# Kernel tuning notes

Hardware: AMD Instinct MI355X
Metric: run time of the kernel (lower is better)

## Reference

```python
import jax, jax.numpy as jnp
import numpy as np

NU, NI, E = 20000, 8000, 64
DV, DT = 4096, 768
NE, B = 200000, 4096
L_HET, L_HOMO = 2, 1
K_ISG, K_UCG = 10, 20
MMW, WD = 0.1, 1e-4


def setup_inputs() -> dict:
    ks = jax.random.split(jax.random.key(0), 14)
    return {
        "feat_v": jax.random.normal(ks[0], (NI, DV), jnp.float32),
        "feat_t": jax.random.normal(ks[1], (NI, DT), jnp.float32),
        "pref_v": jax.random.normal(ks[2], (NU, E), jnp.float32) * 0.1,
        "pref_t": jax.random.normal(ks[3], (NU, E), jnp.float32) * 0.1,
        "W_v": jax.random.normal(ks[4], (DV, E), jnp.float32) * 0.02,
        "W_t": jax.random.normal(ks[5], (DT, E), jnp.float32) * 0.02,
        "user_v_alpha": jax.random.normal(ks[6], (1,), jnp.float32),
        "user_nb_weights": jax.random.normal(ks[7], (NU, K_UCG), jnp.float32),
        "edge_users": jax.random.randint(ks[8], (NE,), 0, NU, jnp.int32),
        "edge_items": jax.random.randint(ks[9], (NE,), 0, NI, jnp.int32),
        "u_ids": jax.random.randint(ks[10], (B,), 0, NU, jnp.int32),
        "pos_ids": jax.random.randint(ks[11], (B,), 0, NI, jnp.int32),
        "neg_ids": jax.random.randint(ks[12], (B,), 0, NI, jnp.int32),
        "user_nb": jax.random.randint(ks[13], (NU, K_UCG), 0, NU, jnp.int32),
    }


def reference(feat_v, feat_t, pref_v, pref_t, W_v, W_t, user_v_alpha,
              user_nb_weights, edge_users, edge_items, u_ids, pos_ids,
              neg_ids, user_nb):
    N = NU + NI
    # bidirectional bipartite edges (items offset by NU)
    src = jnp.concatenate([edge_users, edge_items + NU])
    dst = jnp.concatenate([edge_items + NU, edge_users])
    deg = jax.ops.segment_sum(jnp.ones_like(src, jnp.float32), dst, num_segments=N)
    deg = jnp.maximum(deg, 1.0)
    norm = (1.0 / jnp.sqrt(deg[src] * deg[dst]))[:, None]

    def hetero_gcn(feat, pref, W):
        x = jnp.concatenate([pref, feat @ W], axis=0)  # [N, E]
        h, out = x, x
        for _ in range(L_HET):
            h = jax.ops.segment_sum(h[src] * norm, dst, num_segments=N)
            out = out + h
        return out[:NU], out[NU:]

    u_v, i_v = hetero_gcn(feat_v, pref_v, W_v)
    u_t, i_t = hetero_gcn(feat_t, pref_t, W_t)
    a_v = jax.nn.sigmoid(user_v_alpha[0])
    u_f = jnp.concatenate([a_v * u_v, (1.0 - a_v) * u_t], axis=1)  # [NU, 2E]
    i_f = jnp.concatenate([i_v, i_t], axis=1)                      # [NI, 2E]

    # Item Semantic Graph: KNN over cosine sim, no grad through adjacency.
    def knn_adj(f):
        fn = f / jnp.linalg.norm(f, axis=-1, keepdims=True)
        sim = fn @ fn.T                       # [NI, NI]
        _, idx = jax.lax.top_k(sim, K_ISG)
        return jnp.zeros((NI, NI), f.dtype).at[jnp.arange(NI)[:, None], idx].set(1.0)

    adj = jax.lax.stop_gradient(MMW * knn_adj(feat_v) + (1.0 - MMW) * knn_adj(feat_t))
    rs = adj.sum(axis=1)
    adj = adj * jnp.where(rs > 0, 1.0 / rs, 0.0)[:, None]

    h_i = i_f
    for _ in range(L_HOMO):
        h_i = adj @ h_i

    # User Co-occurrence Graph: scatter-softmax attention aggregation, vectorized.
    attn = jax.nn.softmax(user_nb_weights, axis=1)  # [NU, K]
    h_u = u_f
    for _ in range(L_HOMO):
        h_u = jnp.einsum('uk,ukd->ud', attn, h_u[user_nb])

    z_u = u_f + h_u
    z_i = i_f + h_i
    pos = jnp.sum(z_u[u_ids] * z_i[pos_ids], axis=1)
    neg = jnp.sum(z_u[u_ids] * z_i[neg_ids], axis=1)
    bpr = -jnp.mean(jax.nn.log_sigmoid(pos - neg))
    reg = WD * (jnp.sum(pref_v ** 2) + jnp.sum(pref_t ** 2) + user_v_alpha[0] ** 2) / 2.0
    return bpr + reg
```

## Files before the change

kernel.cpp:

```cpp
#include <hip/hip_runtime.h>
#include <cstdint>
#include <cstddef>

#define NU_C   20000
#define NI_C   8000
#define NTOT_C 28000
#define NE_C   200000
#define B_C    4096
#define NPAD_C 8064
#define NCHUNK 63
#define NPAIR  2016

typedef unsigned short u16;
typedef unsigned int   u32;
typedef unsigned char  u8;
typedef __bf16 bf16x8 __attribute__((ext_vector_type(8)));
typedef float  f32x4  __attribute__((ext_vector_type(4)));

static __device__ __forceinline__ u16 f2bf(float f) {
  u32 u = __float_as_uint(f);
  return (u16)((u + 0x7fffu + ((u >> 16) & 1u)) >> 16);
}

static __device__ __forceinline__ void gl_lds16(const void* g, void* l) {
  __builtin_amdgcn_global_load_lds(
      (const __attribute__((address_space(1))) void*)g,
      (__attribute__((address_space(3))) void*)l, 16, 0, 0);
}

__global__ void conv_kernel2(const float* __restrict__ Fv, const float* __restrict__ Ft,
                             u16* __restrict__ Fbv, u16* __restrict__ Fbt,
                             u8* __restrict__ Fv8,
                             float* __restrict__ rnv, float* __restrict__ rnt) {
  int b = blockIdx.x;
  const int tid = threadIdx.x;
  float ss = 0.f;
  if (b < NPAD_C) {
    const int row = b;
    u16* dst  = Fbv + (size_t)row * 4096;
    u8*  dst8 = Fv8 + (size_t)row * 4096;
    if (row < NI_C) {
      const float* src = Fv + (size_t)row * 4096;
      for (int c = tid * 4; c < 4096; c += 1024) {
        float4 f = *(const float4*)(src + c);
        ss += f.x*f.x + f.y*f.y + f.z*f.z + f.w*f.w;
        ushort4 v; v.x = f2bf(f.x); v.y = f2bf(f.y); v.z = f2bf(f.z); v.w = f2bf(f.w);
        *(ushort4*)(dst + c) = v;
        int w8 = __builtin_amdgcn_cvt_pk_fp8_f32(f.x, f.y, 0, false);
        w8 = __builtin_amdgcn_cvt_pk_fp8_f32(f.z, f.w, w8, true);
        *(u32*)(dst8 + c) = (u32)w8;
      }
    } else {
      for (int c = tid * 4; c < 4096; c += 1024) {
        ushort4 v; v.x = v.y = v.z = v.w = 0;
        *(ushort4*)(dst + c) = v;
        *(u32*)(dst8 + c) = 0u;
      }
    }
    #pragma unroll
    for (int off = 32; off; off >>= 1) ss += __shfl_xor(ss, off);
    __shared__ float red[4];
    if ((tid & 63) == 0) red[tid >> 6] = ss;
    __syncthreads();
    if (tid == 0) {
      float s = red[0] + red[1] + red[2] + red[3];
      rnv[row] = (row < NI_C) ? rsqrtf(s) : 0.f;
    }
  } else {
    const int row = b - NPAD_C;
    u16* dst = Fbt + (size_t)row * 768;
    if (row < NI_C) {
      const float* src = Ft + (size_t)row * 768;
      for (int c = tid * 4; c < 768; c += 1024) {
        float4 f = *(const float4*)(src + c);
        ss += f.x*f.x + f.y*f.y + f.z*f.z + f.w*f.w;
        ushort4 v; v.x = f2bf(f.x); v.y = f2bf(f.y); v.z = f2bf(f.z); v.w = f2bf(f.w);
        *(ushort4*)(dst + c) = v;
      }
    } else {
      for (int c = tid * 4; c < 768; c += 1024) {
        ushort4 v; v.x = v.y = v.z = v.w = 0;
        *(ushort4*)(dst + c) = v;
      }
    }
    #pragma unroll
    for (int off = 32; off; off >>= 1) ss += __shfl_xor(ss, off);
    __shared__ float red[4];
    if ((tid & 63) == 0) red[tid >> 6] = ss;
    __syncthreads();
    if (tid == 0) {
      float s = red[0] + red[1] + red[2] + red[3];
      rnt[row] = (row < NI_C) ? rsqrtf(s) : 0.f;
    }
  }
}

__launch_bounds__(256)
__global__ void simtopk_sym_fp8_kernel(const u8* __restrict__ F, const float* __restrict__ rn,
                                       u32* __restrict__ tv) {
  __shared__ __align__(16) char smem[36864];
  u8*    sB   = (u8*)smem;
  u8*    sA   = (u8*)(smem + 8192);
  float* T    = (float*)smem;
  int*   mk   = (int*)smem;
  int*   mk2  = (int*)(smem + 20480);
  float* sRNI = (float*)(smem + 33792);
  float* sRNJ = (float*)(smem + 34304);

  const int tid  = threadIdx.x;
  const int lane = tid & 63;
  const int wv   = tid >> 6;
  const int n15  = lane & 15;
  const int quad = lane >> 4;

  int I = 0, rem = blockIdx.x;
  { int rowlen = NCHUNK;
    while (rem >= rowlen) { rem -= rowlen; rowlen--; I++; } }
  const int J = I + rem;

  const int l2   = lane >> 2;
  const int lseg = (lane & 3) ^ (l2 & 3) ^ (lane >> 4);
  const u8* gB[2]; const u8* gA[2]; u8* lB[2]; u8* lA[2];
  #pragma unroll
  for (int rep = 0; rep < 2; ++rep) {
    int row = wv * 32 + rep * 16 + l2;
    gB[rep] = F + (size_t)(I * 128 + row) * 4096 + lseg * 16;
    gA[rep] = F + (size_t)(J * 128 + row) * 4096 + lseg * 16;
    lB[rep] = sB + (wv * 32 + rep * 16) * 64;
    lA[rep] = sA + (wv * 32 + rep * 16) * 64;
  }
  const int s_n = (n15 & 3) ^ (n15 >> 2);
  const int q2  = quad >> 1;
  const int q8  = (quad & 1) * 8;
  const int rB0 = (wv * 32 + n15) * 64;
  const int rB1 = rB0 + 16 * 64;

  f32x4 acc[2][8];
  #pragma unroll
  for (int tf = 0; tf < 2; ++tf)
    #pragma unroll
    for (int af = 0; af < 8; ++af) { f32x4 z = {0.f,0.f,0.f,0.f}; acc[tf][af] = z; }

  for (int k0 = 0; k0 < 4096; k0 += 64) {
    __syncthreads();
    gl_lds16(gB[0] + k0, lB[0]);
    gl_lds16(gB[1] + k0, lB[1]);
    gl_lds16(gA[0] + k0, lA[0]);
    gl_lds16(gA[1] + k0, lA[1]);
    if (k0 == 0) {
      if (tid < 128) sRNJ[tid] = rn[J * 128 + tid];
      else           sRNI[tid - 128] = rn[I * 128 + (tid - 128)];
    }
    __syncthreads();
    #pragma unroll
    for (int ks = 0; ks < 2; ++ks) {
      const int sw = (((ks * 2 + q2) ^ s_n) << 4) + q8;
      long long b0 = *(const long long*)(sB + rB0 + sw);
      long long b1 = *(const long long*)(sB + rB1 + sw);
      #pragma unroll
      for (int af = 0; af < 8; ++af) {
        long long a = *(const long long*)(sA + (af * 16 + n15) * 64 + sw);
        acc[0][af] = __builtin_amdgcn_mfma_f32_16x16x32_fp8_fp8(a, b0, acc[0][af], 0, 0, 0);
        acc[1][af] = __builtin_amdgcn_mfma_f32_16x16x32_fp8_fp8(a, b1, acc[1][af], 0, 0, 0);
      }
    }
  }

  int bk[2][10];
  #pragma unroll
  for (int tf = 0; tf < 2; ++tf)
    #pragma unroll
    for (int j = 0; j < 10; ++j) bk[tf][j] = 0;

  #pragma unroll
  for (int af = 0; af < 8; ++af) {
    const float4 rn4 = *(const float4*)(sRNJ + af * 16 + quad * 4);
    const float rna[4] = {rn4.x, rn4.y, rn4.z, rn4.w};
    #pragma unroll
    for (int r = 0; r < 4; ++r) {
      const int ci = J * 128 + af * 16 + quad * 4 + r;
      #pragma unroll
      for (int tf = 0; tf < 2; ++tf) {
        float v = acc[tf][af][r] * rna[r];
        int key = (int)((__float_as_uint(v) & 0xFFFFE000u) | (u32)ci);
        if (ci < NI_C && key > bk[tf][9]) {
          bk[tf][9] = key;
          #pragma unroll
          for (int j = 9; j > 0; --j)
            if (bk[tf][j] > bk[tf][j-1]) { int t = bk[tf][j]; bk[tf][j] = bk[tf][j-1]; bk[tf][j-1] = t; }
        }
      }
    }
  }
  __syncthreads();
  #pragma unroll
  for (int tf = 0; tf < 2; ++tf) {
    int rl = wv * 32 + tf * 16 + n15;
    #pragma unroll
    for (int j = 0; j < 10; ++j) mk[rl * 40 + quad * 10 + j] = bk[tf][j];
  }
  __syncthreads();
  if (tid < 128) {
    int* m = mk + tid * 40;
    int h0 = 0, h1 = 10, h2 = 20, h3 = 30;
    int v0 = m[0], v1 = m[10], v2 = m[20], v3 = m[30];
    #pragma unroll
    for (int s = 0; s < 10; ++s) {
      int m01 = v0 > v1 ? v0 : v1, m23 = v2 > v3 ? v2 : v3;
      int mx = m01 > m23 ? m01 : m23;
      mk2[tid * 10 + s] = mx;
      if      (mx == v0) { ++h0; v0 = (h0 < 10) ? m[h0] : (int)0x80000000; }
      else if (mx == v1) { ++h1; v1 = (h1 < 20) ? m[h1] : (int)0x80000000; }
      else if (mx == v2) { ++h2; v2 = (h2 < 30) ? m[h2] : (int)0x80000000; }
      else               { ++h3; v3 = (h3 < 40) ? m[h3] : (int)0x80000000; }
    }
  }
  __syncthreads();
  { u32* o = tv + ((size_t)J * NPAD_C + I * 128) * 10;
    for (int g = tid; g < 1280; g += 256) o[g] = (u32)mk2[g]; }

  if (I == J) return;

  int bj[2][10];
  #pragma unroll
  for (int s = 0; s < 2; ++s)
    #pragma unroll
    for (int j = 0; j < 10; ++j) bj[s][j] = 0;

  #pragma unroll
  for (int tf = 0; tf < 2; ++tf) {
    __syncthreads();
    #pragma unroll
    for (int af = 0; af < 8; ++af)
      #pragma unroll
      for (int r = 0; r < 4; ++r)
        T[(af * 16 + quad * 4 + r) * 66 + wv * 16 + n15] = acc[tf][af][r];
    __syncthreads();
    #pragma unroll
    for (int s = 0; s < 2; ++s) {
      const int c_own = wv * 32 + s * 16 + n15;
      #pragma unroll
      for (int j = 0; j < 16; ++j) {
        const int t  = quad * 32 + tf * 16 + j;
        const int t64 = quad * 16 + j;
        float v = T[c_own * 66 + t64] * sRNI[t];
        const int ti = I * 128 + t;
        int key = (int)((__float_as_uint(v) & 0xFFFFE000u) | (u32)ti);
        if (ti < NI_C && key > bj[s][9]) {
          bj[s][9] = key;
          #pragma unroll
          for (int q = 9; q > 0; --q)
            if (bj[s][q] > bj[s][q-1]) { int tt = bj[s][q]; bj[s][q] = bj[s][q-1]; bj[s][q-1] = tt; }
        }
      }
    }
  }
  __syncthreads();
  #pragma unroll
  for (int s = 0; s < 2; ++s) {
    int rl = wv * 32 + s * 16 + n15;
    #pragma unroll
    for (int j = 0; j < 10; ++j) mk[rl * 40 + quad * 10 + j] = bj[s][j];
  }
  __syncthreads();
  if (tid < 128) {
    int* m = mk + tid * 40;
    int h0 = 0, h1 = 10, h2 = 20, h3 = 30;
    int v0 = m[0], v1 = m[10], v2 = m[20], v3 = m[30];
    #pragma unroll
    for (int s = 0; s < 10; ++s) {
      int m01 = v0 > v1 ? v0 : v1, m23 = v2 > v3 ? v2 : v3;
      int mx = m01 > m23 ? m01 : m23;
      mk2[tid * 10 + s] = mx;
      if      (mx == v0) { ++h0; v0 = (h0 < 10) ? m[h0] : (int)0x80000000; }
      else if (mx == v1) { ++h1; v1 = (h1 < 20) ? m[h1] : (int)0x80000000; }
      else if (mx == v2) { ++h2; v2 = (h2 < 30) ? m[h2] : (int)0x80000000; }
      else               { ++h3; v3 = (h3 < 40) ? m[h3] : (int)0x80000000; }
    }
  }
  __syncthreads();
  { u32* o = tv + ((size_t)I * NPAD_C + J * 128) * 10;
    for (int g = tid; g < 1280; g += 256) o[g] = (u32)mk2[g]; }
}

template<int D>
__launch_bounds__(256)
__global__ void simtopk_sym_kernel(const u16* __restrict__ F, const float* __restrict__ rn,
                                   u32* __restrict__ tv) {
  __shared__ __align__(16) char smem[40960];
  u16*   sB   = (u16*)smem;
  u16*   sA   = (u16*)(smem + 16384);
  float* T    = (float*)smem;
  int*   mk   = (int*)smem;
  int*   mk2  = (int*)(smem + 20480);
  float* sRNI = (float*)(smem + 34816);
  float* sRNJ = (float*)(smem + 35328);

  const int tid  = threadIdx.x;
  const int lane = tid & 63;
  const int wv   = tid >> 6;
  const int n15  = lane & 15;
  const int quad = lane >> 4;

  int I = 0, rem = blockIdx.x;
  { int rowlen = NCHUNK;
    while (rem >= rowlen) { rem -= rowlen; rowlen--; I++; } }
  const int J = I + rem;

  const int l8  = lane >> 3;
  const int sgu = ((lane & 7) ^ l8) << 3;
  const u16* gB[4]; const u16* gA[4]; u16* lB[4]; u16* lA[4];
  #pragma unroll
  for (int rep = 0; rep < 4; ++rep) {
    int row = wv * 32 + rep * 8 + l8;
    gB[rep] = F + (size_t)(I * 128 + row) * D + sgu;
    gA[rep] = F + (size_t)(J * 128 + row) * D + sgu;
    lB[rep] = sB + wv * 2048 + rep * 512;
    lA[rep] = sA + wv * 2048 + rep * 512;
  }
  const int swu0 = ((quad    ) ^ (n15 & 7)) << 3;
  const int swu1 = ((quad + 4) ^ (n15 & 7)) << 3;
  const int rowB0 = (wv * 32 + n15) * 64;
  const int rowB1 = rowB0 + 16 * 64;

  f32x4 acc[2][8];
  #pragma unroll
  for (int tf = 0; tf < 2; ++tf)
    #pragma unroll
    for (int af = 0; af < 8; ++af) { f32x4 z = {0.f,0.f,0.f,0.f}; acc[tf][af] = z; }

  for (int k0 = 0; k0 < D; k0 += 64) {
    __syncthreads();
    #pragma unroll
    for (int rep = 0; rep < 4; ++rep) gl_lds16(gB[rep] + k0, lB[rep]);
    #pragma unroll
    for (int rep = 0; rep < 4; ++rep) gl_lds16(gA[rep] + k0, lA[rep]);
    if (k0 == 0) {
      if (tid < 128) sRNJ[tid] = rn[J * 128 + tid];
      else           sRNI[tid - 128] = rn[I * 128 + (tid - 128)];
    }
    __syncthreads();
    #pragma unroll
    for (int ks = 0; ks < 2; ++ks) {
      const int swu = ks ? swu1 : swu0;
      bf16x8 b0 = *(const bf16x8*)(sB + rowB0 + swu);
      bf16x8 b1 = *(const bf16x8*)(sB + rowB1 + swu);
      #pragma unroll
      for (int af = 0; af < 8; ++af) {
        bf16x8 a = *(const bf16x8*)(sA + (af * 16 + n15) * 64 + swu);
        acc[0][af] = __builtin_amdgcn_mfma_f32_16x16x32_bf16(a, b0, acc[0][af], 0, 0, 0);
        acc[1][af] = __builtin_amdgcn_mfma_f32_16x16x32_bf16(a, b1, acc[1][af], 0, 0, 0);
      }
    }
  }

  int bk[2][10];
  #pragma unroll
  for (int tf = 0; tf < 2; ++tf)
    #pragma unroll
    for (int j = 0; j < 10; ++j) bk[tf][j] = 0;

  #pragma unroll
  for (int af = 0; af < 8; ++af) {
    const float4 rn4 = *(const float4*)(sRNJ + af * 16 + quad * 4);
    const float rna[4] = {rn4.x, rn4.y, rn4.z, rn4.w};
    #pragma unroll
    for (int r = 0; r < 4; ++r) {
      const int ci = J * 128 + af * 16 + quad * 4 + r;
      #pragma unroll
      for (int tf = 0; tf < 2; ++tf) {
        float v = acc[tf][af][r] * rna[r];
        int key = (int)((__float_as_uint(v) & 0xFFFFE000u) | (u32)ci);
        if (ci < NI_C && key > bk[tf][9]) {
          bk[tf][9] = key;
          #pragma unroll
          for (int j = 9; j > 0; --j)
            if (bk[tf][j] > bk[tf][j-1]) { int t = bk[tf][j]; bk[tf][j] = bk[tf][j-1]; bk[tf][j-1] = t; }
        }
      }
    }
  }
  __syncthreads();
  #pragma unroll
  for (int tf = 0; tf < 2; ++tf) {
    int rl = wv * 32 + tf * 16 + n15;
    #pragma unroll
    for (int j = 0; j < 10; ++j) mk[rl * 40 + quad * 10 + j] = bk[tf][j];
  }
  __syncthreads();
  if (tid < 128) {
    int* m = mk + tid * 40;
    int h0 = 0, h1 = 10, h2 = 20, h3 = 30;
    int v0 = m[0], v1 = m[10], v2 = m[20], v3 = m[30];
    #pragma unroll
    for (int s = 0; s < 10; ++s) {
      int m01 = v0 > v1 ? v0 : v1, m23 = v2 > v3 ? v2 : v3;
      int mx = m01 > m23 ? m01 : m23;
      mk2[tid * 10 + s] = mx;
      if      (mx == v0) { ++h0; v0 = (h0 < 10) ? m[h0] : (int)0x80000000; }
      else if (mx == v1) { ++h1; v1 = (h1 < 20) ? m[h1] : (int)0x80000000; }
      else if (mx == v2) { ++h2; v2 = (h2 < 30) ? m[h2] : (int)0x80000000; }
      else               { ++h3; v3 = (h3 < 40) ? m[h3] : (int)0x80000000; }
    }
  }
  __syncthreads();
  { u32* o = tv + ((size_t)J * NPAD_C + I * 128) * 10;
    for (int g = tid; g < 1280; g += 256) o[g] = (u32)mk2[g]; }

  if (I == J) return;

  int bj[2][10];
  #pragma unroll
  for (int s = 0; s < 2; ++s)
    #pragma unroll
    for (int j = 0; j < 10; ++j) bj[s][j] = 0;

  #pragma unroll
  for (int tf = 0; tf < 2; ++tf) {
    __syncthreads();
    #pragma unroll
    for (int af = 0; af < 8; ++af)
      #pragma unroll
      for (int r = 0; r < 4; ++r)
        T[(af * 16 + quad * 4 + r) * 66 + wv * 16 + n15] = acc[tf][af][r];
    __syncthreads();
    #pragma unroll
    for (int s = 0; s < 2; ++s) {
      const int c_own = wv * 32 + s * 16 + n15;
      #pragma unroll
      for (int j = 0; j < 16; ++j) {
        const int t  = quad * 32 + tf * 16 + j;
        const int t64 = quad * 16 + j;
        float v = T[c_own * 66 + t64] * sRNI[t];
        const int ti = I * 128 + t;
        int key = (int)((__float_as_uint(v) & 0xFFFFE000u) | (u32)ti);
        if (ti < NI_C && key > bj[s][9]) {
          bj[s][9] = key;
          #pragma unroll
          for (int q = 9; q > 0; --q)
            if (bj[s][q] > bj[s][q-1]) { int tt = bj[s][q]; bj[s][q] = bj[s][q-1]; bj[s][q-1] = tt; }
        }
      }
    }
  }
  __syncthreads();
  #pragma unroll
  for (int s = 0; s < 2; ++s) {
    int rl = wv * 32 + s * 16 + n15;
    #pragma unroll
    for (int j = 0; j < 10; ++j) mk[rl * 40 + quad * 10 + j] = bj[s][j];
  }
  __syncthreads();
  if (tid < 128) {
    int* m = mk + tid * 40;
    int h0 = 0, h1 = 10, h2 = 20, h3 = 30;
    int v0 = m[0], v1 = m[10], v2 = m[20], v3 = m[30];
    #pragma unroll
    for (int s = 0; s < 10; ++s) {
      int m01 = v0 > v1 ? v0 : v1, m23 = v2 > v3 ? v2 : v3;
      int mx = m01 > m23 ? m01 : m23;
      mk2[tid * 10 + s] = mx;
      if      (mx == v0) { ++h0; v0 = (h0 < 10) ? m[h0] : (int)0x80000000; }
      else if (mx == v1) { ++h1; v1 = (h1 < 20) ? m[h1] : (int)0x80000000; }
      else if (mx == v2) { ++h2; v2 = (h2 < 30) ? m[h2] : (int)0x80000000; }
      else               { ++h3; v3 = (h3 < 40) ? m[h3] : (int)0x80000000; }
    }
  }
  __syncthreads();
  { u32* o = tv + ((size_t)I * NPAD_C + J * 128) * 10;
    for (int g = tid; g < 1280; g += 256) o[g] = (u32)mk2[g]; }
}

__global__ void merge_topk_kernel(const u32* __restrict__ tv, int* __restrict__ idx) {
  __shared__ int fk[640];
  const int row = blockIdx.x;
  const int tid = threadIdx.x;
  for (int g = tid; g < 630; g += 64)
    fk[g] = (int)tv[((size_t)(g / 10) * NPAD_C + row) * 10 + (g % 10)];
  if (tid < 10) fk[630 + tid] = (int)0x80000000;
  __syncthreads();
  int v[10];
  #pragma unroll
  for (int j = 0; j < 10; ++j) v[j] = fk[tid + j * 64];
  #pragma unroll 1
  for (int s = 0; s < 10; ++s) {
    int loc = v[0];
    #pragma unroll
    for (int j = 1; j < 10; ++j) loc = v[j] > loc ? v[j] : loc;
    #pragma unroll
    for (int off = 32; off; off >>= 1) {
      int o = __shfl_xor(loc, off); loc = o > loc ? o : loc;
    }
    if (tid == 0) idx[row * 10 + s] = loc & 0x1FFF;
    #pragma unroll
    for (int j = 0; j < 10; ++j) if (v[j] == loc) v[j] = (int)0x80000000;
  }
}

__global__ void deg_count_kernel(const int* __restrict__ eu, const int* __restrict__ ei,
                                 float* deg) {
  int e = blockIdx.x * 256 + threadIdx.x;
  if (e < NE_C) {
    atomicAdd(&deg[eu[e]], 1.f);
    atomicAdd(&deg[NU_C + ei[e]], 1.f);
  }
}

__global__ void scan_kernel(float* __restrict__ deg, int* __restrict__ row_start,
                            int* __restrict__ cursor) {
  __shared__ int part[1024];
  const int tid = threadIdx.x;
  const int base = tid * 28;
  float dl[28];
  int local[28];
  int s = 0;
  #pragma unroll
  for (int j = 0; j < 28; ++j) {
    int n = base + j;
    float df = (n < NTOT_C) ? deg[n] : 0.f;
    dl[j] = df;
    local[j] = s; s += (int)df;
  }
  part[tid] = s;
  __syncthreads();
  for (int off = 1; off < 1024; off <<= 1) {
    int v = (tid >= off) ? part[tid - off] : 0;
    __syncthreads();
    part[tid] += v;
    __syncthreads();
  }
  int pre = (tid > 0) ? part[tid - 1] : 0;
  #pragma unroll
  for (int j = 0; j < 28; ++j) {
    int n = base + j;
    if (n < NTOT_C) {
      row_start[n] = pre + local[j];
      cursor[n]    = pre + local[j];
      deg[n]       = rsqrtf(fmaxf(dl[j], 1.f));
    }
  }
  if (tid == 1023) row_start[NTOT_C] = part[1023];
}

__global__ void place_kernel(const int* __restrict__ eu, const int* __restrict__ ei,
                             const float* __restrict__ dinv, int* __restrict__ cursor,
                             int* __restrict__ esrc, float* __restrict__ ew) {
  int e = blockIdx.x * 256 + threadIdx.x;
  if (e >= NE_C) return;
  int u = eu[e], v = NU_C + ei[e];
  float w = dinv[u] * dinv[v];
  int p1 = atomicAdd(&cursor[v], 1);  esrc[p1] = u; ew[p1] = w;
  int p2 = atomicAdd(&cursor[u], 1);  esrc[p2] = v; ew[p2] = w;
}

__global__ void wtrans_kernel(const float* __restrict__ Wv, const float* __restrict__ Wti,
                              u16* __restrict__ Ov, u16* __restrict__ Ot) {
  __shared__ u16 sT[64][72];
  int b = blockIdx.x;
  const float* W; u16* O; int D;
  if (b < 64) { W = Wv; O = Ov; D = 4096; }
  else        { b -= 64; W = Wti; O = Ot; D = 768; }
  const int k0 = b * 64;
  const int r = threadIdx.x >> 6;
  const int c = threadIdx.x & 63;
  for (int rr = r; rr < 64; rr += 4)
    sT[c][rr] = f2bf(W[(size_t)(k0 + rr) * 64 + c]);
  __syncthreads();
  const int n = threadIdx.x >> 2, seg = threadIdx.x & 3;
  uint4 a0 = *(const uint4*)&sT[n][seg * 16];
  uint4 a1 = *(const uint4*)&sT[n][seg * 16 + 8];
  *(uint4*)(O + (size_t)n * D + k0 + seg * 16)     = a0;
  *(uint4*)(O + (size_t)n * D + k0 + seg * 16 + 8) = a1;
}

template<int D>
__launch_bounds__(256)
__global__ void gemm_xw_kernel(const u16* __restrict__ F, const u16* __restrict__ Wt,
                               float* __restrict__ x2, int modeoff) {
  __shared__ __align__(16) u16 sF[64 * 64];
  const int tid  = threadIdx.x;
  const int lane = tid & 63;
  const int wv   = tid >> 6;
  const int n15  = lane & 15;
  const int quad = lane >> 4;
  const int l8   = lane >> 3;
  const int sgu  = ((lane & 7) ^ l8) << 3;
  const u16* gF[2]; u16* lF[2];
  #pragma unroll
  for (int rep = 0; rep < 2; ++rep) {
    int row = rep * 32 + wv * 8 + l8;
    gF[rep] = F + (size_t)(blockIdx.x * 64 + row) * D + sgu;
    lF[rep] = sF + (rep * 32 + wv * 8) * 64;
  }
  const int swu0 = ((quad    ) ^ (n15 & 7)) << 3;
  const int swu1 = ((quad + 4) ^ (n15 & 7)) << 3;

  f32x4 acc[4];
  #pragma unroll
  for (int nf = 0; nf < 4; ++nf) { f32x4 z = {0.f,0.f,0.f,0.f}; acc[nf] = z; }

  for (int k0 = 0; k0 < D; k0 += 64) {
    __syncthreads();
    gl_lds16(gF[0] + k0, lF[0]);
    gl_lds16(gF[1] + k0, lF[1]);
    __syncthreads();
    #pragma unroll
    for (int ks = 0; ks < 2; ++ks) {
      const int swu = ks ? swu1 : swu0;
      bf16x8 a = *(const bf16x8*)(sF + (wv * 16 + n15) * 64 + swu);
      #pragma unroll
      for (int nf = 0; nf < 4; ++nf) {
        bf16x8 b = *(const bf16x8*)(Wt + (size_t)(nf * 16 + n15) * D + k0 + ks * 32 + quad * 8);
        acc[nf] = __builtin_amdgcn_mfma_f32_16x16x32_bf16(a, b, acc[nf], 0, 0, 0);
      }
    }
  }
  #pragma unroll
  for (int nf = 0; nf < 4; ++nf)
    #pragma unroll
    for (int r = 0; r < 4; ++r) {
      int row = blockIdx.x * 64 + wv * 16 + quad * 4 + r;
      if (row < NI_C)
        x2[(size_t)(NU_C + row) * 128 + modeoff + nf * 16 + n15] = acc[nf][r];
    }
}

__global__ void fill_pref_kernel(const float* __restrict__ pv, const float* __restrict__ pt,
                                 float* __restrict__ x2) {
  int gid = blockIdx.x * 256 + threadIdx.x;
  int u = gid >> 7, c = gid & 127;
  x2[gid] = (c < 64) ? pv[(size_t)u * 64 + c] : pt[(size_t)u * 64 + (c - 64)];
}

__global__ void gather2_kernel(const int* __restrict__ row_start, const int* __restrict__ esrc,
                               const float* __restrict__ ew, const float* __restrict__ x2,
                               float* __restrict__ h1) {
  const int node = blockIdx.x * 2 + (threadIdx.x >> 7);
  const int ch   = threadIdx.x & 127;
  if (node >= NTOT_C) return;
  const int b = row_start[node], e = row_start[node + 1];
  float acc = 0.f;
  for (int i = b; i < e; ++i)
    acc += ew[i] * x2[(size_t)esrc[i] * 128 + ch];
  h1[(size_t)node * 128 + ch] = acc;
}

__global__ void gather_comb2_kernel(const int* __restrict__ row_start, const int* __restrict__ esrc,
                                    const float* __restrict__ ew, const float* __restrict__ x2,
                                    const float* __restrict__ h1, const float* __restrict__ alpha,
                                    float* __restrict__ uf, float* __restrict__ ifb) {
  const int node = blockIdx.x * 2 + (threadIdx.x >> 7);
  const int ch   = threadIdx.x & 127;
  if (node >= NTOT_C) return;
  const int b = row_start[node], e = row_start[node + 1];
  float acc = 0.f;
  for (int i = b; i < e; ++i)
    acc += ew[i] * h1[(size_t)esrc[i] * 128 + ch];
  float val = x2[(size_t)node * 128 + ch] + h1[(size_t)node * 128 + ch] + acc;
  if (node < NU_C) {
    float av = 1.f / (1.f + expf(-alpha[0]));
    float coef = (ch < 64) ? av : (1.f - av);
    uf[(size_t)node * 128 + ch] = coef * val;
  } else {
    ifb[(size_t)(node - NU_C) * 128 + ch] = val;
  }
}

__global__ void zuzi_kernel(const float* __restrict__ uf, const float* __restrict__ w,
                            const int* __restrict__ nb, const float* __restrict__ ifb,
                            const int* __restrict__ iv, const int* __restrict__ it,
                            float* __restrict__ zu, float* __restrict__ zi) {
  const int c = threadIdx.x;
  if (blockIdx.x < NU_C) {
    const int u = blockIdx.x;
    __shared__ float at[20];
    if (c < 20) at[c] = w[u * 20 + c];
    __syncthreads();
    float e[20]; float m = -1e30f;
    #pragma unroll
    for (int k = 0; k < 20; ++k) { e[k] = at[k]; m = fmaxf(m, e[k]); }
    float ssum = 0.f;
    #pragma unroll
    for (int k = 0; k < 20; ++k) { e[k] = expf(e[k] - m); ssum += e[k]; }
    float inv = 1.f / ssum;
    float acc = 0.f;
    #pragma unroll
    for (int k = 0; k < 20; ++k) {
      int j = nb[u * 20 + k];
      acc += e[k] * inv * uf[(size_t)j * 128 + c];
    }
    zu[(size_t)u * 128 + c] = uf[(size_t)u * 128 + c] + acc;
  } else {
    const int i = blockIdx.x - NU_C;
    float sv = 0.f, st = 0.f;
    #pragma unroll
    for (int k = 0; k < 10; ++k) sv += ifb[(size_t)iv[i * 10 + k] * 128 + c];
    #pragma unroll
    for (int k = 0; k < 10; ++k) st += ifb[(size_t)it[i * 10 + k] * 128 + c];
    zi[(size_t)i * 128 + c] = ifb[(size_t)i * 128 + c] + 0.01f * sv + 0.09f * st;
  }
}

__global__ void loss_kernel(const float* __restrict__ zu, const float* __restrict__ zi,
                            const int* __restrict__ uid, const int* __restrict__ pid,
                            const int* __restrict__ nid, const float* __restrict__ pv,
                            const float* __restrict__ pt, const float* __restrict__ alpha,
                            float* __restrict__ out) {
  if (blockIdx.x < 1024) {
    int wv = threadIdx.x >> 6, lane = threadIdx.x & 63;
    int b = blockIdx.x * 4 + wv;
    int u = uid[b], p = pid[b], n = nid[b];
    float2 a  = *(const float2*)(zu + (size_t)u * 128 + lane * 2);
    float2 xp = *(const float2*)(zi + (size_t)p * 128 + lane * 2);
    float2 xn = *(const float2*)(zi + (size_t)n * 128 + lane * 2);
    float d = a.x * (xp.x - xn.x) + a.y * (xp.y - xn.y);
    #pragma unroll
    for (int off = 32; off; off >>= 1) d += __shfl_xor(d, off);
    if (lane == 0) {
      float xv = -d;
      float sp = fmaxf(xv, 0.f) + log1pf(expf(-fabsf(xv)));
      atomicAdd(out, sp * (1.f / (float)B_C));
    }
  } else {
    const size_t N1 = (size_t)NU_C * 64;
    float acc = 0.f;
    for (size_t i = (size_t)(blockIdx.x - 1024) * 256 + threadIdx.x; i < 2 * N1;
         i += (size_t)512 * 256) {
      float x = (i < N1) ? pv[i] : pt[i - N1];
      acc += x * x;
    }
    #pragma unroll
    for (int off = 32; off; off >>= 1) acc += __shfl_xor(acc, off);
    __shared__ float red[4];
    if ((threadIdx.x & 63) == 0) red[threadIdx.x >> 6] = acc;
    __syncthreads();
    if (threadIdx.x == 0) {
      float s = red[0] + red[1] + red[2] + red[3];
      atomicAdd(out, 0.5e-4f * s);
    }
    if (blockIdx.x == 1024 && threadIdx.x == 0) {
      float a = alpha[0];
      atomicAdd(out, 0.5e-4f * a * a);
    }
  }
}

extern "C" void kernel_launch(void* const* d_in, const int* in_sizes, int n_in,
                              void* d_out, int out_size, void* d_ws, size_t ws_size,
                              hipStream_t stream) {
  const float* feat_v = (const float*)d_in[0];
  const float* feat_t = (const float*)d_in[1];
  const float* pref_v = (const float*)d_in[2];
  const float* pref_t = (const float*)d_in[3];
  const float* W_v    = (const float*)d_in[4];
  const float* W_t    = (const float*)d_in[5];
  const float* alpha  = (const float*)d_in[6];
  const float* unw    = (const float*)d_in[7];
  const int* eu       = (const int*)d_in[8];
  const int* ei       = (const int*)d_in[9];
  const int* u_ids    = (const int*)d_in[10];
  const int* pos_ids  = (const int*)d_in[11];
  const int* neg_ids  = (const int*)d_in[12];
  const int* user_nb  = (const int*)d_in[13];
  float* out = (float*)d_out;
  char* ws = (char*)d_ws;

  size_t off = 0;
  auto alloc = [&](size_t bytes) { char* p = ws + off; off += (bytes + 255) & ~(size_t)255; return p; };
  u16*   fvbf  = (u16*)alloc((size_t)NPAD_C * 4096 * 2);
  u8*    fv8   = (u8*)alloc((size_t)NPAD_C * 4096);
  u16*   ftbf  = (u16*)alloc((size_t)NPAD_C * 768 * 2);
  u16*   wtv   = (u16*)alloc((size_t)64 * 4096 * 2);
  u16*   wtt   = (u16*)alloc((size_t)64 * 768 * 2);
  float* rn_v  = (float*)alloc(NPAD_C * 4);
  float* rn_t  = (float*)alloc(NPAD_C * 4);
  int*   idx_v = (int*)alloc(NI_C * 10 * 4);
  int*   idx_t = (int*)alloc(NI_C * 10 * 4);
  float* dinv  = (float*)alloc(NTOT_C * 4);
  int*   rowst = (int*)alloc((NTOT_C + 1) * 4);
  int*   curs  = (int*)alloc(NTOT_C * 4);
  int*   esrc  = (int*)alloc((size_t)2 * NE_C * 4);
  float* ew    = (float*)alloc((size_t)2 * NE_C * 4);
  float* x2    = (float*)alloc((size_t)NTOT_C * 128 * 4);
  float* h1    = (float*)alloc((size_t)NTOT_C * 128 * 4);
  char*  pC    = alloc((size_t)(NU_C + NI_C) * 128 * 4 * 2);
  u32*   tvb   = (u32*)pC;
  float* u_f   = (float*)pC;
  float* i_f   = (float*)(pC + (size_t)NU_C * 128 * 4);
  float* z_u   = (float*)(pC + (size_t)(NU_C + NI_C) * 128 * 4);
  float* z_i   = (float*)(pC + (size_t)(2 * NU_C + NI_C) * 128 * 4);

  hipMemsetAsync(out, 0, sizeof(float), stream);
  hipMemsetAsync(dinv, 0, NTOT_C * 4, stream);

  deg_count_kernel<<<(NE_C + 255) / 256, 256, 0, stream>>>(eu, ei, dinv);
  scan_kernel<<<1, 1024, 0, stream>>>(dinv, rowst, curs);
  place_kernel<<<(NE_C + 255) / 256, 256, 0, stream>>>(eu, ei, dinv, curs, esrc, ew);

  conv_kernel2<<<2 * NPAD_C, 256, 0, stream>>>(feat_v, feat_t, fvbf, ftbf, fv8, rn_v, rn_t);
  wtrans_kernel<<<76, 256, 0, stream>>>(W_v, W_t, wtv, wtt);

  simtopk_sym_fp8_kernel<<<NPAIR, 256, 0, stream>>>(fv8, rn_v, tvb);
  merge_topk_kernel<<<NI_C, 64, 0, stream>>>(tvb, idx_v);
  simtopk_sym_kernel<768><<<NPAIR, 256, 0, stream>>>(ftbf, rn_t, tvb);
  merge_topk_kernel<<<NI_C, 64, 0, stream>>>(tvb, idx_t);

  fill_pref_kernel<<<(NU_C * 128) / 256, 256, 0, stream>>>(pref_v, pref_t, x2);
  gemm_xw_kernel<4096><<<125, 256, 0, stream>>>(fvbf, wtv, x2, 0);
  gemm_xw_kernel<768><<<125, 256, 0, stream>>>(ftbf, wtt, x2, 64);
  gather2_kernel<<<14000, 256, 0, stream>>>(rowst, esrc, ew, x2, h1);
  gather_comb2_kernel<<<14000, 256, 0, stream>>>(rowst, esrc, ew, x2, h1, alpha, u_f, i_f);

  zuzi_kernel<<<NU_C + NI_C, 128, 0, stream>>>(u_f, unw, user_nb, i_f, idx_v, idx_t, z_u, z_i);
  loss_kernel<<<1536, 256, 0, stream>>>(z_u, z_i, u_ids, pos_ids, neg_ids,
                                        pref_v, pref_t, alpha, out);
}
```

Baseline: 1.124 ms.

## Double-buffer LDS tiles in the fp8 similarity top-k GEMM loop

```diff
diff --git a/kernel.cpp b/kernel.cpp
--- a/kernel.cpp
+++ b/kernel.cpp
@@ -98,9 +98,7 @@
 __launch_bounds__(256)
 __global__ void simtopk_sym_fp8_kernel(const u8* __restrict__ F, const float* __restrict__ rn,
                                        u32* __restrict__ tv) {
-  __shared__ __align__(16) char smem[36864];
-  u8*    sB   = (u8*)smem;
-  u8*    sA   = (u8*)(smem + 8192);
+  __shared__ __align__(16) char smem[34816];
   float* T    = (float*)smem;
   int*   mk   = (int*)smem;
   int*   mk2  = (int*)(smem + 20480);
@@ -120,49 +118,67 @@
 
   const int l2   = lane >> 2;
   const int lseg = (lane & 3) ^ (l2 & 3) ^ (lane >> 4);
-  const u8* gB[2]; const u8* gA[2]; u8* lB[2]; u8* lA[2];
+  const u8* gB[2]; const u8* gA[2];
   #pragma unroll
   for (int rep = 0; rep < 2; ++rep) {
     int row = wv * 32 + rep * 16 + l2;
     gB[rep] = F + (size_t)(I * 128 + row) * 4096 + lseg * 16;
     gA[rep] = F + (size_t)(J * 128 + row) * 4096 + lseg * 16;
-    lB[rep] = sB + (wv * 32 + rep * 16) * 64;
-    lA[rep] = sA + (wv * 32 + rep * 16) * 64;
-  }
+  }
+  const int oB0 = wv * 2048;
+  const int oB1 = wv * 2048 + 1024;
+  const int oA0 = 8192 + wv * 2048;
+  const int oA1 = 8192 + wv * 2048 + 1024;
   const int s_n = (n15 & 3) ^ (n15 >> 2);
   const int q2  = quad >> 1;
   const int q8  = (quad & 1) * 8;
   const int rB0 = (wv * 32 + n15) * 64;
   const int rB1 = rB0 + 16 * 64;
 
+  auto stage = [&](int p, int k0) {
+    u8* base = (u8*)smem + p * 16384;
+    gl_lds16(gB[0] + k0, base + oB0);
+    gl_lds16(gB[1] + k0, base + oB1);
+    gl_lds16(gA[0] + k0, base + oA0);
+    gl_lds16(gA[1] + k0, base + oA1);
+  };
+
   f32x4 acc[2][8];
   #pragma unroll
   for (int tf = 0; tf < 2; ++tf)
     #pragma unroll
     for (int af = 0; af < 8; ++af) { f32x4 z = {0.f,0.f,0.f,0.f}; acc[tf][af] = z; }
 
-  for (int k0 = 0; k0 < 4096; k0 += 64) {
-    __syncthreads();
-    gl_lds16(gB[0] + k0, lB[0]);
-    gl_lds16(gB[1] + k0, lB[1]);
-    gl_lds16(gA[0] + k0, lA[0]);
-    gl_lds16(gA[1] + k0, lA[1]);
-    if (k0 == 0) {
-      if (tid < 128) sRNJ[tid] = rn[J * 128 + tid];
-      else           sRNI[tid - 128] = rn[I * 128 + (tid - 128)];
-    }
-    __syncthreads();
+  if (tid < 128) sRNJ[tid] = rn[J * 128 + tid];
+  else           sRNI[tid - 128] = rn[I * 128 + (tid - 128)];
+  asm volatile("s_waitcnt lgkmcnt(0)" ::: "memory");
+  stage(0, 0);
+  asm volatile("s_waitcnt vmcnt(0)" ::: "memory");
+  __builtin_amdgcn_s_barrier();
+
+  int cur = 0;
+  for (int t = 0; t < 64; ++t) {
+    if (t < 63) stage(cur ^ 1, (t + 1) * 64);
+    const u8* sBp = (const u8*)smem + cur * 16384;
+    const u8* sAp = sBp + 8192;
+    __builtin_amdgcn_s_setprio(1);
     #pragma unroll
     for (int ks = 0; ks < 2; ++ks) {
       const int sw = (((ks * 2 + q2) ^ s_n) << 4) + q8;
-      long long b0 = *(const long long*)(sB + rB0 + sw);
-      long long b1 = *(const long long*)(sB + rB1 + sw);
+      long long b0 = *(const long long*)(sBp + rB0 + sw);
+      long long b1 = *(const long long*)(sBp + rB1 + sw);
       #pragma unroll
       for (int af = 0; af < 8; ++af) {
-        long long a = *(const long long*)(sA + (af * 16 + n15) * 64 + sw);
+        long long a = *(const long long*)(sAp + (af * 16 + n15) * 64 + sw);
         acc[0][af] = __builtin_amdgcn_mfma_f32_16x16x32_fp8_fp8(a, b0, acc[0][af], 0, 0, 0);
         acc[1][af] = __builtin_amdgcn_mfma_f32_16x16x32_fp8_fp8(a, b1, acc[1][af], 0, 0, 0);
       }
+    }
+    __builtin_amdgcn_s_setprio(0);
+    if (t < 63) {
+      asm volatile("s_waitcnt vmcnt(0)" ::: "memory");
+      __builtin_amdgcn_s_barrier();
+      cur ^= 1;
     }
   }
 
```

Measured after the change: 1.160 ms. +3.3%, slower.
